# Kernel optimization log

Hardware: AMD Instinct MI355X
Metric: run time of the kernel (lower is better)

## Reference

```python
import jax, jax.numpy as jnp
import numpy as np

# ---- dimensions ----
N = 16384      # nodes
E = 131072     # edges (avg degree 8)
F = 128        # scalar channel width == s_dim
L = 9          # spherical-harmonic components (lmax=2)
R = 8          # radial basis size
DOUT = L * F   # post-product node width (1152)
K = 1024       # fixed number of master nodes (static stand-in for m>0.5)
HID = 64       # master-selection hidden dim
DA = 64        # virtual-attention head dim
LAMBDA_ATTN = 0.5
R_CUT = 5.0
EPS = 1e-9


def sh_l2(u):
    # real SH polynomials up to l=2 on unit vectors u[..., 3] -> [..., 9]
    x, y, z = u[..., 0], u[..., 1], u[..., 2]
    o = jnp.ones_like(x)
    return jnp.stack([o, x, y, z, x * y, y * z, 3.0 * z * z - 1.0, x * z, x * x - y * y], axis=-1)


def bessel(r):
    # Bessel radial basis; r [..., 1] -> [..., R]
    n = jnp.arange(1, R + 1, dtype=r.dtype)
    return jnp.sqrt(2.0 / R_CUT) * jnp.sin(n * jnp.pi * r / R_CUT) / jnp.maximum(r, EPS)


def setup_inputs() -> dict:
    key = jax.random.key(0)
    ks = jax.random.split(key, 18)
    s = lambda d: 1.0 / np.sqrt(d)
    return {
        'h': jax.random.normal(ks[0], (N, F), jnp.float32),
        'pos': 3.0 * jax.random.normal(ks[1], (N, 3), jnp.float32),
        'edge_sh': jax.random.normal(ks[2], (E, L), jnp.float32),
        'edge_feats': jax.random.uniform(ks[3], (E, R), jnp.float32),
        'W_node_l': s(F) * jax.random.normal(ks[4], (F, F), jnp.float32),
        'W_rad_l': s(R) * jax.random.normal(ks[5], (R, F), jnp.float32),
        'W_prod_l': s(L * F) * jax.random.normal(ks[6], (L, F, DOUT), jnp.float32),
        'ms_W1': s(F) * jax.random.normal(ks[7], (F, HID), jnp.float32),
        'ms_b1': jnp.zeros((HID,), jnp.float32),
        'ms_W2': s(HID) * jax.random.normal(ks[8], (HID, 1), jnp.float32),
        'ms_b2': jnp.zeros((1,), jnp.float32),
        'vg_Wq': s(F) * jax.random.normal(ks[9], (F, DA), jnp.float32),
        'vg_Wk': s(F) * jax.random.normal(ks[10], (F, DA), jnp.float32),
        'W_node_h': s(DOUT) * jax.random.normal(ks[11], (DOUT, F), jnp.float32),
        'W_rad_h': s(R) * jax.random.normal(ks[12], (R, F), jnp.float32),
        'W_prod_h': s(L * F) * jax.random.normal(ks[13], (L, F, DOUT), jnp.float32),
        'edge_index': jax.random.randint(ks[14], (2, E), 0, N),
    }


def reference(h, pos, edge_sh, edge_feats, W_node_l, W_rad_l, W_prod_l,
              ms_W1, ms_b1, ms_W2, ms_b2, vg_Wq, vg_Wk,
              W_node_h, W_rad_h, W_prod_h, edge_index):
    src, dst = edge_index[0], edge_index[1]

    # ---- local conv + reshape + prod (with padded residual sc) ----
    t = (h[src] @ W_node_l) * (edge_feats @ W_rad_l)                      # [E,F]
    msg = edge_sh[:, :, None] * t[:, None, :]                             # [E,L,F]
    upd = jax.ops.segment_sum(msg, dst, num_segments=N)                   # [N,L,F]
    sc = jnp.pad(h, ((0, 0), (0, DOUT - F)))
    h_local = jnp.einsum('nlf,lfg->ng', upd, W_prod_l) + sc               # [N,DOUT]

    # ---- master selection (MLP -> sigmoid); fixed top-K masters ----
    hs = h_local[:, :F]
    m = jax.nn.sigmoid(jax.nn.relu(hs @ ms_W1 + ms_b1) @ ms_W2 + ms_b2)[:, 0]  # [N]
    _, midx = jax.lax.top_k(m, K)
    master_idx = jnp.sort(midx)                                           # [K]

    # ---- induced subgraph among masters as dense [K,K] adjacency ----
    rank = jnp.full((N,), K, dtype=jnp.int32).at[master_idx].set(jnp.arange(K, dtype=jnp.int32))
    adj = jnp.zeros((K + 1, K + 1), h.dtype).at[rank[src], rank[dst]].max(jnp.ones((E,), h.dtype))
    adj_induced = adj[:K, :K]

    h_m = h_local[master_idx]                                             # [K,DOUT]
    pos_m = pos[master_idx]                                               # [K,3]
    hms = h_m[:, :F]

    # ---- virtual graph generation (attention -> thresholded dense adj) ----
    q = hms @ vg_Wq
    kk = hms @ vg_Wk
    A = jax.nn.sigmoid(q @ kk.T / jnp.sqrt(jnp.asarray(DA, h.dtype)))     # [K,K]
    A_virtual = jnp.where(A > LAMBDA_ATTN, A, 0.0)
    eye = jnp.eye(K, dtype=bool)
    Bv = (A_virtual > 0) & ~eye                                           # remove self loops
    Bv = Bv | Bv.T                                                        # to_undirected
    adj_master = jnp.clip(adj_induced + Bv.astype(h.dtype), 0.0, 1.0) * (1.0 - jnp.eye(K, dtype=h.dtype))

    # ---- hierarchical conv over dense master graph ----
    A_rec = adj_master.T                                                  # A_rec[i,j]=1: sender j -> receiver i
    V = pos_m[None, :, :] - pos_m[:, None, :]                             # vec = pos[src]-pos[dst]
    r = jnp.linalg.norm(V, axis=-1, keepdims=True)                        # [K,K,1]
    u = V / jnp.maximum(r, EPS)
    sh_m = sh_l2(u)                                                       # [K,K,L]
    rad = bessel(r)                                                       # [K,K,R]
    tm = (h_m @ W_node_h)[None, :, :] * (rad @ W_rad_h) * A_rec[:, :, None]  # [K,K,F]
    upd_m = jnp.einsum('ijl,ijf->ilf', sh_m, tm)                          # [K,L,F]
    h_hier = jnp.einsum('ilf,lfg->ig', upd_m, W_prod_h) + h_m             # sc_master pad is 0-width

    # ---- masked scatter blend ----
    h_exp = jnp.zeros_like(h_local).at[master_idx].set(h_hier)
    h_final = (1.0 - m[:, None]) * h_local + m[:, None] * h_exp
    return (h_final, A_virtual, m, master_idx)
```

## Files before the change

kernel.cpp:

```cpp
#include <hip/hip_runtime.h>
#include <hip/hip_bf16.h>
#include <stdint.h>

#define N_NODES 16384
#define E_EDGES 131072
#define F_DIM 128
#define L_DIM 9
#define R_DIM 8
#define DOUT_DIM 1152
#define K_SEL 1024
#define HID_DIM 64
#define DA_DIM 64

typedef unsigned short u16;
typedef __attribute__((ext_vector_type(8))) short bf16x8;
typedef __attribute__((ext_vector_type(4))) float f32x4;

static __device__ inline u16 f2bs(float x) {
  union { __hip_bfloat16 b; u16 s; } u;
  u.b = __float2bfloat16(x);
  return u.s;
}

#define GLDS16(gsrc, ldst) __builtin_amdgcn_global_load_lds( \
    (__attribute__((address_space(1))) void*)(void*)(gsrc),  \
    (__attribute__((address_space(3))) void*)(ldst), 16, 0, 0)

__global__ __launch_bounds__(256) void gemm_mfma(
    const float* __restrict__ A, const u16* __restrict__ Bt,
    float* __restrict__ C, int ldc, int M, int Nc, int Kc,
    const float* __restrict__ Add, int ldadd, int addW)
{
  __shared__ float Af[128 * 32];
  __shared__ u16  Bs[128 * 32];
  const int tid = threadIdx.x;
  const int wave = tid >> 6, lane = tid & 63;
  const int wm = wave >> 1, wn = wave & 1;
  const int l15 = lane & 15, quad = lane >> 4;
  const int bm = blockIdx.y * 128, bn = blockIdx.x * 128;

  f32x4 acc[4][4];
#pragma unroll
  for (int i = 0; i < 4; i++)
#pragma unroll
    for (int j = 0; j < 4; j++) acc[i][j] = (f32x4)(0.f);

  for (int k0 = 0; k0 < Kc; k0 += 32) {
    __syncthreads();
#pragma unroll
    for (int it = 0; it < 4; it++) {
      int c = it * 256 + tid;
      int row = c >> 3, op = c & 7;
      int oct = op ^ (row & 7);
      const float* g = A + (size_t)(bm + row) * Kc + k0 + oct * 4;
      GLDS16(g, &Af[c * 4]);
    }
#pragma unroll
    for (int it = 0; it < 2; it++) {
      int c = it * 256 + tid;
      int row = c >> 2, qp = c & 3;
      int q = qp ^ ((row >> 1) & 3);
      const u16* g = Bt + (size_t)(bn + row) * Kc + k0 + q * 8;
      GLDS16(g, &Bs[c * 8]);
    }
    __syncthreads();

    bf16x8 af[4], bfg[4];
#pragma unroll
    for (int mi = 0; mi < 4; mi++) {
      int m = wm * 64 + mi * 16 + l15;
      int o0 = (quad * 2) ^ (m & 7), o1 = (quad * 2 + 1) ^ (m & 7);
      float4 lo = *(const float4*)&Af[m * 32 + o0 * 4];
      float4 hi = *(const float4*)&Af[m * 32 + o1 * 4];
      bf16x8 r;
      r[0] = (short)f2bs(lo.x); r[1] = (short)f2bs(lo.y);
      r[2] = (short)f2bs(lo.z); r[3] = (short)f2bs(lo.w);
      r[4] = (short)f2bs(hi.x); r[5] = (short)f2bs(hi.y);
      r[6] = (short)f2bs(hi.z); r[7] = (short)f2bs(hi.w);
      af[mi] = r;
    }
#pragma unroll
    for (int ni = 0; ni < 4; ni++) {
      int n = wn * 64 + ni * 16 + l15;
      int q2 = quad ^ ((n >> 1) & 3);
      bfg[ni] = *(const bf16x8*)&Bs[n * 32 + q2 * 8];
    }
#pragma unroll
    for (int mi = 0; mi < 4; mi++)
#pragma unroll
      for (int ni = 0; ni < 4; ni++)
        acc[mi][ni] = __builtin_amdgcn_mfma_f32_16x16x32_bf16(af[mi], bfg[ni], acc[mi][ni], 0, 0, 0);
  }
#pragma unroll
  for (int mi = 0; mi < 4; mi++)
#pragma unroll
    for (int ni = 0; ni < 4; ni++)
#pragma unroll
      for (int r = 0; r < 4; r++) {
        int row = bm + wm * 64 + mi * 16 + quad * 4 + r;
        int col = bn + wn * 64 + ni * 16 + l15;
        float v = acc[mi][ni][r];
        if (Add != nullptr && col < addW) v += Add[(size_t)row * ldadd + col];
        C[(size_t)row * ldc + col] = v;
      }
}

__global__ __launch_bounds__(256) void gemm_mfma_b16(
    const u16* __restrict__ A, const u16* __restrict__ Bt,
    float* __restrict__ C, int ldc, int Kc, int nbx, int nwg,
    const float* __restrict__ Add, int ldadd, int addW)
{
  __shared__ u16 As[128 * 32];
  __shared__ u16 Bs[128 * 32];
  const int tid = threadIdx.x;
  const int wave = tid >> 6, lane = tid & 63;
  const int wm = wave >> 1, wn = wave & 1;
  const int l15 = lane & 15, quad = lane >> 4;
  const int lin = blockIdx.x;
  const int swz = (lin & 7) * (nwg >> 3) + (lin >> 3);
  const int bm = (swz / nbx) * 128, bn = (swz % nbx) * 128;

  f32x4 acc[4][4];
#pragma unroll
  for (int i = 0; i < 4; i++)
#pragma unroll
    for (int j = 0; j < 4; j++) acc[i][j] = (f32x4)(0.f);

  for (int k0 = 0; k0 < Kc; k0 += 32) {
    __syncthreads();
#pragma unroll
    for (int it = 0; it < 2; it++) {
      int c = it * 256 + tid;
      int row = c >> 2, qp = c & 3;
      int q = qp ^ ((row >> 1) & 3);
      const u16* g = A + (size_t)(bm + row) * Kc + k0 + q * 8;
      GLDS16(g, &As[c * 8]);
    }
#pragma unroll
    for (int it = 0; it < 2; it++) {
      int c = it * 256 + tid;
      int row = c >> 2, qp = c & 3;
      int q = qp ^ ((row >> 1) & 3);
      const u16* g = Bt + (size_t)(bn + row) * Kc + k0 + q * 8;
      GLDS16(g, &Bs[c * 8]);
    }
    __syncthreads();

    bf16x8 af[4], bfg[4];
#pragma unroll
    for (int mi = 0; mi < 4; mi++) {
      int m = wm * 64 + mi * 16 + l15;
      af[mi] = *(const bf16x8*)&As[m * 32 + (quad ^ ((m >> 1) & 3)) * 8];
    }
#pragma unroll
    for (int ni = 0; ni < 4; ni++) {
      int n = wn * 64 + ni * 16 + l15;
      bfg[ni] = *(const bf16x8*)&Bs[n * 32 + (quad ^ ((n >> 1) & 3)) * 8];
    }
#pragma unroll
    for (int mi = 0; mi < 4; mi++)
#pragma unroll
      for (int ni = 0; ni < 4; ni++)
        acc[mi][ni] = __builtin_amdgcn_mfma_f32_16x16x32_bf16(af[mi], bfg[ni], acc[mi][ni], 0, 0, 0);
  }
#pragma unroll
  for (int mi = 0; mi < 4; mi++)
#pragma unroll
    for (int ni = 0; ni < 4; ni++)
#pragma unroll
      for (int r = 0; r < 4; r++) {
        int row = bm + wm * 64 + mi * 16 + quad * 4 + r;
        int col = bn + wn * 64 + ni * 16 + l15;
        float v = acc[mi][ni][r];
        if (Add != nullptr && col < addW) v += Add[(size_t)row * ldadd + col];
        C[(size_t)row * ldc + col] = v;
      }
}

__global__ __launch_bounds__(256) void transpose_bf16(
    const float* __restrict__ W, u16* __restrict__ Bt, int K, int N)
{
  __shared__ float t[32][33];
  const int n0 = blockIdx.x * 32, k0 = blockIdx.y * 32;
  const int tx = threadIdx.x & 31, ty = threadIdx.x >> 5;
  for (int r = ty; r < 32; r += 8) t[r][tx] = W[(size_t)(k0 + r) * N + n0 + tx];
  __syncthreads();
  for (int r = ty; r < 32; r += 8) Bt[(size_t)(n0 + r) * K + k0 + tx] = f2bs(t[tx][r]);
}

#define BM 128
#define BN 128
#define BK 16
__global__ __launch_bounds__(256) void gemm_f32(
    const float* __restrict__ A, int lda,
    const float* __restrict__ B, int ldb,
    float* __restrict__ C, int ldc,
    int M, int Nc, int Kc,
    const float* __restrict__ Add, int ldadd, int addW)
{
  __shared__ float As[BK][BM + 1];
  __shared__ float Bs[BK][BN];
  const int tid = threadIdx.x;
  const int tx = tid & 15, ty = tid >> 4;
  const int bm = blockIdx.y * BM, bn = blockIdx.x * BN;
  float acc[8][8];
#pragma unroll
  for (int i = 0; i < 8; i++)
#pragma unroll
    for (int j = 0; j < 8; j++) acc[i][j] = 0.f;
  for (int k0 = 0; k0 < Kc; k0 += BK) {
    const int ac = tid & 15, ar0 = tid >> 4;
#pragma unroll
    for (int rr = 0; rr < 8; rr++) {
      int row = ar0 + rr * 16;
      As[ac][row] = A[(size_t)(bm + row) * lda + k0 + ac];
    }
    const int bc = tid & 127, br0 = tid >> 7;
#pragma unroll
    for (int rr = 0; rr < 8; rr++) {
      int kr = br0 + rr * 2;
      Bs[kr][bc] = B[(size_t)(k0 + kr) * ldb + bn + bc];
    }
    __syncthreads();
#pragma unroll
    for (int kk = 0; kk < BK; kk++) {
      float a[8], b[8];
#pragma unroll
      for (int i = 0; i < 8; i++) a[i] = As[kk][ty * 8 + i];
#pragma unroll
      for (int j = 0; j < 8; j++) b[j] = Bs[kk][tx * 8 + j];
#pragma unroll
      for (int i = 0; i < 8; i++)
#pragma unroll
        for (int j = 0; j < 8; j++) acc[i][j] = fmaf(a[i], b[j], acc[i][j]);
    }
    __syncthreads();
  }
#pragma unroll
  for (int i = 0; i < 8; i++) {
    int row = bm + ty * 8 + i;
#pragma unroll
    for (int j = 0; j < 8; j++) {
      int col = bn + tx * 8 + j;
      float v = acc[i][j];
      if (Add != nullptr && col < addW) v += Add[(size_t)row * ldadd + col];
      C[(size_t)row * ldc + col] = v;
    }
  }
}

__global__ __launch_bounds__(256) void gemm64_f32(
    const float* __restrict__ A, int lda,
    const float* __restrict__ B, int ldb,
    float* __restrict__ C, int ldc,
    int M, int Nc, int Kc, int kPerSplit,
    const float* __restrict__ Add, int ldadd, int addW)
{
  __shared__ float As[16][65];
  __shared__ float Bs[16][64];
  const int tid = threadIdx.x;
  const int tx = tid & 15, ty = tid >> 4;
  const int bm = blockIdx.y * 64, bn = blockIdx.x * 64;
  const int kb = blockIdx.z * kPerSplit;
  const int ke = min(kb + kPerSplit, Kc);
  float acc[4][4];
#pragma unroll
  for (int i = 0; i < 4; i++)
#pragma unroll
    for (int j = 0; j < 4; j++) acc[i][j] = 0.f;
  for (int k0 = kb; k0 < ke; k0 += 16) {
    const int ac = tid & 15, ar = tid >> 4;
#pragma unroll
    for (int rr = 0; rr < 4; rr++) {
      int row = ar + rr * 16;
      As[ac][row] = A[(size_t)(bm + row) * lda + k0 + ac];
    }
    const int bc = tid & 63, br = tid >> 6;
#pragma unroll
    for (int rr = 0; rr < 4; rr++) {
      int kr = br + rr * 4;
      Bs[kr][bc] = B[(size_t)(k0 + kr) * ldb + bn + bc];
    }
    __syncthreads();
#pragma unroll
    for (int kk = 0; kk < 16; kk++) {
      float a[4], b[4];
#pragma unroll
      for (int i = 0; i < 4; i++) a[i] = As[kk][ty * 4 + i];
#pragma unroll
      for (int j = 0; j < 4; j++) b[j] = Bs[kk][tx * 4 + j];
#pragma unroll
      for (int i = 0; i < 4; i++)
#pragma unroll
        for (int j = 0; j < 4; j++) acc[i][j] = fmaf(a[i], b[j], acc[i][j]);
    }
    __syncthreads();
  }
#pragma unroll
  for (int i = 0; i < 4; i++) {
    int row = bm + ty * 4 + i;
#pragma unroll
    for (int j = 0; j < 4; j++) {
      int col = bn + tx * 4 + j;
      if (gridDim.z > 1) {
        atomicAdd(&C[(size_t)row * ldc + col], acc[i][j]);
      } else {
        float v = acc[i][j];
        if (Add != nullptr && col < addW) v += Add[(size_t)row * ldadd + col];
        C[(size_t)row * ldc + col] = v;
      }
    }
  }
}

__global__ __launch_bounds__(256) void count_kernel(
    const int* __restrict__ ei, int* __restrict__ counts)
{
  int e = blockIdx.x * 256 + threadIdx.x;
  atomicAdd(&counts[ei[E_EDGES + e]], 1);
}

__global__ __launch_bounds__(1024) void scan_kernel(
    const int* __restrict__ counts, int* __restrict__ offsets, int* __restrict__ cursor)
{
  __shared__ int part[1024];
  const int t = threadIdx.x;
  const int base = t * 16;
  int loc[16];
  int s = 0;
#pragma unroll
  for (int k = 0; k < 16; k++) { loc[k] = counts[base + k]; s += loc[k]; }
  part[t] = s;
  __syncthreads();
  for (int d = 1; d < 1024; d <<= 1) {
    int v = (t >= d) ? part[t - d] : 0;
    __syncthreads();
    part[t] += v;
    __syncthreads();
  }
  int run = part[t] - s;
#pragma unroll
  for (int k = 0; k < 16; k++) {
    offsets[base + k] = run;
    cursor[base + k] = run;
    run += loc[k];
  }
}

__global__ __launch_bounds__(256) void fill_kernel(
    const int* __restrict__ ei, int* __restrict__ cursor, int* __restrict__ elist)
{
  int e = blockIdx.x * 256 + threadIdx.x;
  int d = ei[E_EDGES + e];
  int p = atomicAdd(&cursor[d], 1);
  elist[p] = e;
}

__global__ __launch_bounds__(128) void gather_accum_kernel(
    const float* __restrict__ hW, const float* __restrict__ edge_sh,
    const float* __restrict__ edge_feats, const float* __restrict__ W_rad_l,
    const int* __restrict__ ei, const int* __restrict__ offsets,
    const int* __restrict__ counts, const int* __restrict__ elist,
    float* __restrict__ upd, u16* __restrict__ updb)
{
  __shared__ float sWr[R_DIM * F_DIM];
  const int d = blockIdx.x, f = threadIdx.x;
  for (int t = f; t < R_DIM * F_DIM; t += 128) sWr[t] = W_rad_l[t];
  __syncthreads();
  const int b = offsets[d], n = counts[d];
  float acc[L_DIM];
#pragma unroll
  for (int l = 0; l < L_DIM; l++) acc[l] = 0.f;
  for (int k = 0; k < n; k++) {
    const int e = elist[b + k];
    const int s = ei[e];
    float rw = 0.f;
#pragma unroll
    for (int p = 0; p < R_DIM; p++)
      rw = fmaf(edge_feats[(size_t)e * R_DIM + p], sWr[p * F_DIM + f], rw);
    const float tf = hW[(size_t)s * F_DIM + f] * rw;
#pragma unroll
    for (int l = 0; l < L_DIM; l++)
      acc[l] = fmaf(edge_sh[(size_t)e * L_DIM + l], tf, acc[l]);
  }
#pragma unroll
  for (int l = 0; l < L_DIM; l++)
    upd[(size_t)d * DOUT_DIM + l * F_DIM + f] = acc[l];
  if (updb != nullptr) {
#pragma unroll
    for (int l = 0; l < L_DIM; l++)
      updb[(size_t)d * DOUT_DIM + l * F_DIM + f] = f2bs(acc[l]);
  }
}

__global__ __launch_bounds__(256) void gate_kernel(
    const float* __restrict__ hs, const float* __restrict__ W1,
    const float* __restrict__ b1, const float* __restrict__ W2,
    const float* __restrict__ b2, float* __restrict__ m_ws, float* __restrict__ m_out,
    int* __restrict__ hist1)
{
  __shared__ float sW1[F_DIM * HID_DIM];
  __shared__ float srow[4][F_DIM];
  const int tid = threadIdx.x;
  for (int t = tid; t < F_DIM * HID_DIM; t += 256) sW1[t] = W1[t];
  const int wave = tid >> 6, lane = tid & 63;
  const int n = blockIdx.x * 4 + wave;
  srow[wave][lane] = hs[(size_t)n * F_DIM + lane];
  srow[wave][lane + 64] = hs[(size_t)n * F_DIM + lane + 64];
  __syncthreads();
  float hid = b1[lane];
#pragma unroll 8
  for (int c = 0; c < F_DIM; c++) hid = fmaf(srow[wave][c], sW1[c * HID_DIM + lane], hid);
  hid = fmaxf(hid, 0.f);
  float v = hid * W2[lane];
#pragma unroll
  for (int off = 32; off > 0; off >>= 1) v += __shfl_down(v, off);
  if (lane == 0) {
    float mm = 1.f / (1.f + expf(-(v + b2[0])));
    m_ws[n] = mm;
    m_out[n] = mm;
    unsigned mb = __float_as_uint(mm);
    atomicAdd(&hist1[mb >> 16], 1);
  }
}

__global__ __launch_bounds__(1024) void radix_sel_kernel(
    const int* __restrict__ hist, const int* __restrict__ kin, int kinIdx,
    int* __restrict__ outp, int outIdx)
{
  __shared__ int part[1024];
  const int t = threadIdx.x;
  const int Kv = kin ? kin[kinIdx] : K_SEL;
  const int base = t * 64;
  int s = 0;
  for (int k = 0; k < 64; k++) s += hist[base + k];
  part[t] = s;
  __syncthreads();
  for (int d = 1; d < 1024; d <<= 1) {
    int v = (t + d < 1024) ? part[t + d] : 0;
    __syncthreads();
    part[t] += v;
    __syncthreads();
  }
  int inc = part[t];
  if (inc >= Kv && inc - s < Kv) {
    int r = inc - s;
    for (int b = base + 63; b >= base; b--) {
      int hv = hist[b];
      if (r + hv >= Kv) { outp[outIdx] = b; outp[outIdx + 1] = Kv - r; break; }
      r += hv;
    }
  }
}

__global__ __launch_bounds__(256) void hist2_kernel(
    const float* __restrict__ m_ws, const int* __restrict__ selb, int* __restrict__ hist2)
{
  int i = blockIdx.x * 256 + threadIdx.x;
  unsigned mb = __float_as_uint(m_ws[i]);
  if ((int)(mb >> 16) == selb[0]) atomicAdd(&hist2[mb & 0xFFFFu], 1);
}

__global__ __launch_bounds__(256) void flag_kernel(
    const float* __restrict__ m_ws, int* __restrict__ selb,
    unsigned char* __restrict__ flags, int* __restrict__ cand)
{
  int i = blockIdx.x * 256 + threadIdx.x;
  unsigned mb = __float_as_uint(m_ws[i]);
  unsigned vb = ((unsigned)selb[0] << 16) | (unsigned)selb[2];
  unsigned char fl = 0;
  if (mb > vb) fl = 1;
  else if (mb == vb) { int p = atomicAdd(&selb[4], 1); cand[p] = i; }
  flags[i] = fl;
}

__global__ __launch_bounds__(1024) void cand_kernel(
    const int* __restrict__ selb, const int* __restrict__ cand, unsigned char* __restrict__ flags)
{
  const int nc = selb[4], need = selb[3];
  for (int c = threadIdx.x; c < nc; c += 1024) {
    const int idx = cand[c];
    int r = 0;
    for (int o = 0; o < nc; o++) r += (cand[o] < idx) ? 1 : 0;
    if (r < need) flags[idx] = 1;
  }
}

__global__ __launch_bounds__(1024) void compact_kernel(
    const unsigned char* __restrict__ flags, int* __restrict__ midx,
    int* __restrict__ rank, float* __restrict__ mi_out)
{
  __shared__ int part[1024];
  const int t = threadIdx.x;
  const int base = t * 16;
  int loc[16];
  int s = 0;
#pragma unroll
  for (int k = 0; k < 16; k++) { loc[k] = flags[base + k]; s += loc[k]; }
  part[t] = s;
  __syncthreads();
  for (int d = 1; d < 1024; d <<= 1) {
    int v = (t >= d) ? part[t - d] : 0;
    __syncthreads();
    part[t] += v;
    __syncthreads();
  }
  int run = part[t] - s;
#pragma unroll
  for (int k = 0; k < 16; k++) {
    int i = base + k;
    if (loc[k]) {
      midx[run] = i;
      mi_out[run] = (float)i;
      rank[i] = run;
      run++;
    } else {
      rank[i] = K_SEL;
    }
  }
}

__global__ __launch_bounds__(256) void adj_kernel(
    const int* __restrict__ ei, const int* __restrict__ rank, unsigned char* __restrict__ adjm)
{
  int e = blockIdx.x * 256 + threadIdx.x;
  int rs = rank[ei[e]];
  int rd = rank[ei[E_EDGES + e]];
  if (rs < K_SEL && rd < K_SEL) adjm[(size_t)rs * K_SEL + rd] = 1;
}

__global__ __launch_bounds__(128) void gather_kernel(
    const float* __restrict__ hl, const float* __restrict__ pos,
    const int* __restrict__ midx, float* __restrict__ h_m, float* __restrict__ pos_m)
{
  const int rI = blockIdx.x, t = threadIdx.x;
  const int mi = midx[rI];
  const float4* src = (const float4*)(hl + (size_t)mi * DOUT_DIM);
  float4* dst = (float4*)(h_m + (size_t)rI * DOUT_DIM);
  for (int c = t; c < DOUT_DIM / 4; c += 128) dst[c] = src[c];
  if (t < 3) pos_m[rI * 3 + t] = pos[mi * 3 + t];
}

__global__ __launch_bounds__(128) void qk_kernel(
    const float* __restrict__ hs, const int* __restrict__ midx,
    const float* __restrict__ Wq, const float* __restrict__ Wk,
    float* __restrict__ q, float* __restrict__ kk)
{
  __shared__ float row[F_DIM];
  const int i = blockIdx.x, t = threadIdx.x;
  const int mi = midx[i];
  row[t] = hs[(size_t)mi * F_DIM + t];
  __syncthreads();
  const int d = t & 63;
  const float* W = (t < 64) ? Wq : Wk;
  float acc = 0.f;
#pragma unroll 8
  for (int c = 0; c < F_DIM; c++) acc = fmaf(row[c], W[c * DA_DIM + d], acc);
  float* dst = (t < 64) ? q : kk;
  dst[(size_t)i * DA_DIM + d] = acc;
}

__global__ __launch_bounds__(256) void attn_kernel(
    const float* __restrict__ q, const float* __restrict__ kk,
    unsigned char* __restrict__ maskA, float* __restrict__ Av)
{
  __shared__ float qs[16][DA_DIM], ks[16][DA_DIM];
  const int tx = threadIdx.x, ty = threadIdx.y;
  const int tid = ty * 16 + tx;
  const int i0 = blockIdx.y * 16, j0 = blockIdx.x * 16;
  for (int t = tid; t < 16 * DA_DIM; t += 256) {
    int rr = t >> 6, cc = t & 63;
    qs[rr][cc] = q[(size_t)(i0 + rr) * DA_DIM + cc];
    ks[rr][cc] = kk[(size_t)(j0 + rr) * DA_DIM + cc];
  }
  __syncthreads();
  float acc = 0.f;
#pragma unroll
  for (int d2 = 0; d2 < DA_DIM; d2++) acc = fmaf(qs[ty][d2], ks[tx][d2], acc);
  float sgl = 1.f / (1.f + expf(-acc * 0.125f));
  size_t o = (size_t)(i0 + ty) * K_SEL + (j0 + tx);
  bool big = sgl > 0.5f;
  maskA[o] = big ? 1 : 0;
  Av[o] = big ? sgl : 0.f;
}

__global__ __launch_bounds__(256) void listbuild_kernel(
    const unsigned char* __restrict__ adjm, const unsigned char* __restrict__ maskA,
    u16* __restrict__ list, int* __restrict__ nj)
{
  __shared__ int cnt;
  const int i = blockIdx.x, tid = threadIdx.x;
  if (tid == 0) cnt = 0;
  __syncthreads();
#pragma unroll
  for (int jt = 0; jt < 4; jt++) {
    int j = jt * 256 + tid;
    bool e = (j != i) && (adjm[(size_t)j * K_SEL + i] | maskA[(size_t)j * K_SEL + i] |
                          maskA[(size_t)i * K_SEL + j]);
    if (e) {
      int p = atomicAdd(&cnt, 1);
      list[(size_t)i * K_SEL + p] = (u16)j;
    }
  }
  __syncthreads();
  if (tid == 0) nj[i] = cnt;
}

__global__ __launch_bounds__(512) void hier2_kernel(
    const float* __restrict__ hWn, const float* __restrict__ pos_m,
    const float* __restrict__ W_rad_h, const u16* __restrict__ list,
    const int* __restrict__ nj, float* __restrict__ upd_m, u16* __restrict__ updb_m)
{
  __shared__ float sW[R_DIM * F_DIM];
  __shared__ float gsm[128][20];
  __shared__ int sj[128];
  __shared__ float red[3][L_DIM][F_DIM];
  const int tid = threadIdx.x;
  const int i = blockIdx.x;
  const int f = tid & 127, jsub = tid >> 7;
  for (int t = tid; t < R_DIM * F_DIM; t += 512) sW[t] = W_rad_h[t];
  const float pix = pos_m[i * 3 + 0], piy = pos_m[i * 3 + 1], piz = pos_m[i * 3 + 2];
  float acc[L_DIM];
#pragma unroll
  for (int l = 0; l < L_DIM; l++) acc[l] = 0.f;
  const int n = nj[i];
  for (int c0 = 0; c0 < n; c0 += 128) {
    const int cnt = min(128, n - c0);
    __syncthreads();
    if (tid < cnt) {
      const int j = list[(size_t)i * K_SEL + c0 + tid];
      sj[tid] = j;
      float vx = pos_m[j * 3 + 0] - pix;
      float vy = pos_m[j * 3 + 1] - piy;
      float vz = pos_m[j * 3 + 2] - piz;
      float r = sqrtf(vx * vx + vy * vy + vz * vz);
      float rm = fmaxf(r, 1e-9f);
      float inv = 1.f / rm;
      float ux = vx * inv, uy = vy * inv, uz = vz * inv;
      gsm[tid][0] = 1.f; gsm[tid][1] = ux; gsm[tid][2] = uy; gsm[tid][3] = uz;
      gsm[tid][4] = ux * uy; gsm[tid][5] = uy * uz;
      gsm[tid][6] = 3.f * uz * uz - 1.f;
      gsm[tid][7] = ux * uz; gsm[tid][8] = ux * ux - uy * uy;
      float theta = 0.62831853071795864769f * r;
      float s1 = sinf(theta), c1 = cosf(theta);
      float coef = 0.632455532033675866f * inv;
      float snm2 = 0.f, snm1 = s1;
      gsm[tid][9] = s1 * coef;
#pragma unroll
      for (int nn = 2; nn <= R_DIM; nn++) {
        float sn = 2.f * c1 * snm1 - snm2;
        gsm[tid][8 + nn] = sn * coef;
        snm2 = snm1; snm1 = sn;
      }
      gsm[tid][17] = 0.f; gsm[tid][18] = 0.f; gsm[tid][19] = 0.f;
    }
    __syncthreads();
    for (int t = jsub; t < cnt; t += 4) {
      const int j = sj[t];
      const float hw = hWn[(size_t)j * F_DIM + f];
      float4 g0 = *(const float4*)&gsm[t][0];
      float4 g1 = *(const float4*)&gsm[t][4];
      float4 g2 = *(const float4*)&gsm[t][8];
      float4 g3 = *(const float4*)&gsm[t][12];
      float  g4 = gsm[t][16];
      float rw = g2.y * sW[0 * F_DIM + f];
      rw = fmaf(g2.z, sW[1 * F_DIM + f], rw);
      rw = fmaf(g2.w, sW[2 * F_DIM + f], rw);
      rw = fmaf(g3.x, sW[3 * F_DIM + f], rw);
      rw = fmaf(g3.y, sW[4 * F_DIM + f], rw);
      rw = fmaf(g3.z, sW[5 * F_DIM + f], rw);
      rw = fmaf(g3.w, sW[6 * F_DIM + f], rw);
      rw = fmaf(g4,   sW[7 * F_DIM + f], rw);
      const float tm = hw * rw;
      acc[0] = fmaf(g0.x, tm, acc[0]); acc[1] = fmaf(g0.y, tm, acc[1]);
      acc[2] = fmaf(g0.z, tm, acc[2]); acc[3] = fmaf(g0.w, tm, acc[3]);
      acc[4] = fmaf(g1.x, tm, acc[4]); acc[5] = fmaf(g1.y, tm, acc[5]);
      acc[6] = fmaf(g1.z, tm, acc[6]); acc[7] = fmaf(g1.w, tm, acc[7]);
      acc[8] = fmaf(g2.x, tm, acc[8]);
    }
  }
  __syncthreads();
  if (jsub > 0) {
#pragma unroll
    for (int l = 0; l < L_DIM; l++) red[jsub - 1][l][f] = acc[l];
  }
  __syncthreads();
  if (jsub == 0) {
#pragma unroll
    for (int l = 0; l < L_DIM; l++) {
      float v = acc[l] + red[0][l][f] + red[1][l][f] + red[2][l][f];
      upd_m[(size_t)i * DOUT_DIM + l * F_DIM + f] = v;
      updb_m[(size_t)i * DOUT_DIM + l * F_DIM + f] = f2bs(v);
    }
  }
}

__global__ __launch_bounds__(256) void combine_kernel(
    float* __restrict__ out0, const float* __restrict__ h_hier,
    const float* __restrict__ m_ws, const int* __restrict__ rank)
{
  size_t i4 = (size_t)blockIdx.x * 256 + threadIdx.x;
  int n = (int)(i4 / (DOUT_DIM / 4));
  int g4 = (int)(i4 % (DOUT_DIM / 4));
  float mv = m_ws[n];
  int r = rank[n];
  float4 hl = ((const float4*)out0)[i4];
  float4 he = make_float4(0.f, 0.f, 0.f, 0.f);
  if (r < K_SEL) he = ((const float4*)h_hier)[(size_t)r * (DOUT_DIM / 4) + g4];
  float4 o;
  o.x = (1.f - mv) * hl.x + mv * he.x;
  o.y = (1.f - mv) * hl.y + mv * he.y;
  o.z = (1.f - mv) * hl.z + mv * he.z;
  o.w = (1.f - mv) * hl.w + mv * he.w;
  ((float4*)out0)[i4] = o;
}

extern "C" void kernel_launch(void* const* d_in, const int* in_sizes, int n_in,
                              void* d_out, int out_size, void* d_ws, size_t ws_size,
                              hipStream_t stream)
{
  const float* h         = (const float*)d_in[0];
  const float* pos       = (const float*)d_in[1];
  const float* edge_sh   = (const float*)d_in[2];
  const float* edge_feats= (const float*)d_in[3];
  const float* W_node_l  = (const float*)d_in[4];
  const float* W_rad_l   = (const float*)d_in[5];
  const float* W_prod_l  = (const float*)d_in[6];
  const float* ms_W1     = (const float*)d_in[7];
  const float* ms_b1     = (const float*)d_in[8];
  const float* ms_W2     = (const float*)d_in[9];
  const float* ms_b2     = (const float*)d_in[10];
  const float* vg_Wq     = (const float*)d_in[11];
  const float* vg_Wk     = (const float*)d_in[12];
  const float* W_node_h  = (const float*)d_in[13];
  const float* W_rad_h   = (const float*)d_in[14];
  const float* W_prod_h  = (const float*)d_in[15];
  const int*   eidx      = (const int*)d_in[16];

  float* out    = (float*)d_out;
  float* out_hf = out;
  float* out_Av = out + (size_t)N_NODES * DOUT_DIM;
  float* out_m  = out_Av + (size_t)K_SEL * K_SEL;
  float* out_mi = out_m + N_NODES;

  char* ws = (char*)d_ws;
  float* upd = (float*)ws;
  float* hW  = (float*)(ws + (size_t)N_NODES * DOUT_DIM * 4);
  float* hs  = hW;
  const size_t updbOff = (size_t)N_NODES * DOUT_DIM * 4 + (size_t)N_NODES * F_DIM * 4;
  const size_t updbNeed = updbOff + (size_t)N_NODES * DOUT_DIM * 2;
  const bool useB16 = (ws_size >= updbNeed);
  u16* updb = (u16*)(ws + updbOff);
  u16* Btl = (u16*)out_Av;
  char* csr = (char*)out_Av + (((size_t)DOUT_DIM * DOUT_DIM * 2 + 255) & ~(size_t)255);
  int* counts  = (int*)csr;
  int* offsets = counts + N_NODES;
  int* cursor  = offsets + N_NODES;
  int* elist   = cursor + N_NODES;
  size_t off = 0;
  auto alloc = [&](size_t bytes) -> void* {
    void* p = ws + off;
    off += (bytes + 255) & ~(size_t)255;
    return p;
  };
  float* m_ws  = (float*)alloc((size_t)N_NODES * 4);
  int*   rank  = (int*)alloc((size_t)N_NODES * 4);
  int*   midx  = (int*)alloc((size_t)K_SEL * 4);
  int*   hist1 = (int*)alloc((size_t)65536 * 4);
  int*   hist2 = (int*)alloc((size_t)65536 * 4);
  int*   selb  = (int*)alloc((size_t)64 * 4);
  int*   cand  = (int*)alloc((size_t)N_NODES * 4);
  unsigned char* flags = (unsigned char*)alloc((size_t)N_NODES);
  unsigned char* adjm  = (unsigned char*)alloc((size_t)K_SEL * K_SEL);
  unsigned char* maskA = (unsigned char*)alloc((size_t)K_SEL * K_SEL);
  float* qbuf  = (float*)alloc((size_t)K_SEL * DA_DIM * 4);
  float* kbuf  = (float*)alloc((size_t)K_SEL * DA_DIM * 4);
  float* h_m   = (float*)alloc((size_t)K_SEL * DOUT_DIM * 4);
  float* pos_m = (float*)alloc((size_t)K_SEL * 3 * 4);
  float* hWn   = (float*)alloc((size_t)K_SEL * F_DIM * 4);
  float* upd_m = (float*)alloc((size_t)K_SEL * DOUT_DIM * 4);
  float* h_hier= (float*)alloc((size_t)K_SEL * DOUT_DIM * 4);
  u16*   Bth   = (u16*)alloc((size_t)DOUT_DIM * DOUT_DIM * 2);
  u16*   jlist = (u16*)alloc((size_t)K_SEL * K_SEL * 2);
  int*   njbuf = (int*)alloc((size_t)K_SEL * 4);
  u16*   updbm = (u16*)alloc((size_t)K_SEL * DOUT_DIM * 2);

  hipMemsetAsync(counts, 0, (size_t)N_NODES * 4, stream);
  transpose_bf16<<<dim3(DOUT_DIM / 32, DOUT_DIM / 32), 256, 0, stream>>>(
      W_prod_l, Btl, DOUT_DIM, DOUT_DIM);
  gemm_f32<<<dim3(1, N_NODES / 128), 256, 0, stream>>>(
      h, F_DIM, W_node_l, F_DIM, hW, F_DIM, N_NODES, F_DIM, F_DIM, nullptr, 0, 0);
  count_kernel<<<E_EDGES / 256, 256, 0, stream>>>(eidx, counts);
  scan_kernel<<<1, 1024, 0, stream>>>(counts, offsets, cursor);
  fill_kernel<<<E_EDGES / 256, 256, 0, stream>>>(eidx, cursor, elist);
  gather_accum_kernel<<<N_NODES, 128, 0, stream>>>(
      hW, edge_sh, edge_feats, W_rad_l, eidx, offsets, counts, elist, upd,
      useB16 ? updb : nullptr);
  gemm64_f32<<<dim3(F_DIM / 64, N_NODES / 64, 1), 256, 0, stream>>>(
      upd, DOUT_DIM, W_prod_l, DOUT_DIM, hs, F_DIM,
      N_NODES, F_DIM, DOUT_DIM, DOUT_DIM, h, F_DIM, F_DIM);
  if (useB16) {
    gemm_mfma_b16<<<(DOUT_DIM / 128) * (N_NODES / 128), 256, 0, stream>>>(
        updb, Btl, out_hf, DOUT_DIM, DOUT_DIM, DOUT_DIM / 128,
        (DOUT_DIM / 128) * (N_NODES / 128), h, F_DIM, F_DIM);
  } else {
    gemm_mfma<<<dim3(DOUT_DIM / 128, N_NODES / 128), 256, 0, stream>>>(
        upd, Btl, out_hf, DOUT_DIM, N_NODES, DOUT_DIM, DOUT_DIM, h, F_DIM, F_DIM);
  }

  hipMemsetAsync(adjm, 0, (size_t)K_SEL * K_SEL, stream);
  hipMemsetAsync(hist1, 0, (size_t)65536 * 4 * 2 + 256, stream);
  transpose_bf16<<<dim3(DOUT_DIM / 32, DOUT_DIM / 32), 256, 0, stream>>>(
      W_prod_h, Bth, DOUT_DIM, DOUT_DIM);
  gate_kernel<<<N_NODES / 4, 256, 0, stream>>>(hs, ms_W1, ms_b1, ms_W2, ms_b2,
                                               m_ws, out_m, hist1);
  radix_sel_kernel<<<1, 1024, 0, stream>>>(hist1, nullptr, 0, selb, 0);
  hist2_kernel<<<N_NODES / 256, 256, 0, stream>>>(m_ws, selb, hist2);
  radix_sel_kernel<<<1, 1024, 0, stream>>>(hist2, selb, 1, selb, 2);
  flag_kernel<<<N_NODES / 256, 256, 0, stream>>>(m_ws, selb, flags, cand);
  cand_kernel<<<1, 1024, 0, stream>>>(selb, cand, flags);
  compact_kernel<<<1, 1024, 0, stream>>>(flags, midx, rank, out_mi);
  adj_kernel<<<E_EDGES / 256, 256, 0, stream>>>(eidx, rank, adjm);
  gather_kernel<<<K_SEL, 128, 0, stream>>>(out_hf, pos, midx, h_m, pos_m);
  qk_kernel<<<K_SEL, 128, 0, stream>>>(hs, midx, vg_Wq, vg_Wk, qbuf, kbuf);
  attn_kernel<<<dim3(K_SEL / 16, K_SEL / 16), dim3(16, 16), 0, stream>>>(qbuf, kbuf, maskA, out_Av);
  listbuild_kernel<<<K_SEL, 256, 0, stream>>>(adjm, maskA, jlist, njbuf);
  hipMemsetAsync(hWn, 0, (size_t)K_SEL * F_DIM * 4, stream);
  gemm64_f32<<<dim3(F_DIM / 64, K_SEL / 64, 4), 256, 0, stream>>>(
      h_m, DOUT_DIM, W_node_h, F_DIM, hWn, F_DIM,
      K_SEL, F_DIM, DOUT_DIM, DOUT_DIM / 4, nullptr, 0, 0);
  hier2_kernel<<<K_SEL, 512, 0, stream>>>(hWn, pos_m, W_rad_h, jlist, njbuf, upd_m, updbm);
  gemm_mfma_b16<<<(DOUT_DIM / 128) * (K_SEL / 128), 256, 0, stream>>>(
      updbm, Bth, h_hier, DOUT_DIM, DOUT_DIM, DOUT_DIM / 128,
      (DOUT_DIM / 128) * (K_SEL / 128), h_m, DOUT_DIM, DOUT_DIM);
  combine_kernel<<<(N_NODES * DOUT_DIM / 4) / 256, 256, 0, stream>>>(out_hf, h_hier, m_ws, rank);
}
```

Before: 734.2 us.

## Split-K the hs projection GEMM with 128x128 tiles and a reduce pass

Replaces the 64x64-tile fp32 GEMM that computes hs (the first 128 output columns, using upd and W_prod_l) with a 128x128-tile kernel split four ways along K. Partial sums go to the not-yet-written output buffer, and a separate vectorized kernel sums the four partials and adds the h residual. The small h@W_node_l GEMM now uses the 64x64 kernel instead of the 128-tile one, which gives it more blocks. The split-K path is meant to raise per-thread reuse and parallelism, and in exchange adds an extra 32 MB write and read of partials and one more launch.

```diff
diff --git a/kernel.cpp b/kernel.cpp
--- a/kernel.cpp
+++ b/kernel.cpp
@@ -188,42 +188,39 @@
   for (int r = ty; r < 32; r += 8) Bt[(size_t)(n0 + r) * K + k0 + tx] = f2bs(t[tx][r]);
 }
 
-#define BM 128
-#define BN 128
-#define BK 16
-__global__ __launch_bounds__(256) void gemm_f32(
-    const float* __restrict__ A, int lda,
-    const float* __restrict__ B, int ldb,
-    float* __restrict__ C, int ldc,
-    int M, int Nc, int Kc,
-    const float* __restrict__ Add, int ldadd, int addW)
-{
-  __shared__ float As[BK][BM + 1];
-  __shared__ float Bs[BK][BN];
+__global__ __launch_bounds__(256) void hs_gemm_kernel(
+    const float* __restrict__ A,
+    const float* __restrict__ B,
+    float* __restrict__ psum)
+{
+  __shared__ float As[16][129];
+  __shared__ float Bs[16][128];
   const int tid = threadIdx.x;
   const int tx = tid & 15, ty = tid >> 4;
-  const int bm = blockIdx.y * BM, bn = blockIdx.x * BN;
+  const int bm = blockIdx.x * 128;
+  const int z = blockIdx.y;
+  const int kb = z * (DOUT_DIM / 4);
   float acc[8][8];
 #pragma unroll
   for (int i = 0; i < 8; i++)
 #pragma unroll
     for (int j = 0; j < 8; j++) acc[i][j] = 0.f;
-  for (int k0 = 0; k0 < Kc; k0 += BK) {
+  for (int k0 = kb; k0 < kb + DOUT_DIM / 4; k0 += 16) {
     const int ac = tid & 15, ar0 = tid >> 4;
 #pragma unroll
     for (int rr = 0; rr < 8; rr++) {
       int row = ar0 + rr * 16;
-      As[ac][row] = A[(size_t)(bm + row) * lda + k0 + ac];
+      As[ac][row] = A[(size_t)(bm + row) * DOUT_DIM + k0 + ac];
     }
     const int bc = tid & 127, br0 = tid >> 7;
 #pragma unroll
     for (int rr = 0; rr < 8; rr++) {
       int kr = br0 + rr * 2;
-      Bs[kr][bc] = B[(size_t)(k0 + kr) * ldb + bn + bc];
-    }
-    __syncthreads();
-#pragma unroll
-    for (int kk = 0; kk < BK; kk++) {
+      Bs[kr][bc] = B[(size_t)(k0 + kr) * DOUT_DIM + bc];
+    }
+    __syncthreads();
+#pragma unroll
+    for (int kk = 0; kk < 16; kk++) {
       float a[8], b[8];
 #pragma unroll
       for (int i = 0; i < 8; i++) a[i] = As[kk][ty * 8 + i];
@@ -238,15 +235,27 @@
   }
 #pragma unroll
   for (int i = 0; i < 8; i++) {
-    int row = bm + ty * 8 + i;
-#pragma unroll
-    for (int j = 0; j < 8; j++) {
-      int col = bn + tx * 8 + j;
-      float v = acc[i][j];
-      if (Add != nullptr && col < addW) v += Add[(size_t)row * ldadd + col];
-      C[(size_t)row * ldc + col] = v;
-    }
-  }
+    size_t row = (size_t)z * N_NODES + bm + ty * 8 + i;
+#pragma unroll
+    for (int j = 0; j < 8; j++)
+      psum[row * F_DIM + tx * 8 + j] = acc[i][j];
+  }
+}
+
+__global__ __launch_bounds__(256) void hs_reduce_kernel(
+    const float* __restrict__ psum, const float* __restrict__ h, float* __restrict__ hs)
+{
+  size_t i4 = (size_t)blockIdx.x * 256 + threadIdx.x;
+  const size_t stride = (size_t)N_NODES * F_DIM / 4;
+  const float4* p = (const float4*)psum;
+  float4 a = p[i4], b = p[i4 + stride], c = p[i4 + 2 * stride], d = p[i4 + 3 * stride];
+  float4 hh = ((const float4*)h)[i4];
+  float4 o;
+  o.x = a.x + b.x + c.x + d.x + hh.x;
+  o.y = a.y + b.y + c.y + d.y + hh.y;
+  o.z = a.z + b.z + c.z + d.z + hh.z;
+  o.w = a.w + b.w + c.w + d.w + hh.w;
+  ((float4*)hs)[i4] = o;
 }
 
 __global__ __launch_bounds__(256) void gemm64_f32(
@@ -751,6 +760,7 @@
   const size_t updbNeed = updbOff + (size_t)N_NODES * DOUT_DIM * 2;
   const bool useB16 = (ws_size >= updbNeed);
   u16* updb = (u16*)(ws + updbOff);
+  float* psum = out_hf;
   u16* Btl = (u16*)out_Av;
   char* csr = (char*)out_Av + (((size_t)DOUT_DIM * DOUT_DIM * 2 + 255) & ~(size_t)255);
   int* counts  = (int*)csr;
@@ -788,17 +798,16 @@
   hipMemsetAsync(counts, 0, (size_t)N_NODES * 4, stream);
   transpose_bf16<<<dim3(DOUT_DIM / 32, DOUT_DIM / 32), 256, 0, stream>>>(
       W_prod_l, Btl, DOUT_DIM, DOUT_DIM);
-  gemm_f32<<<dim3(1, N_NODES / 128), 256, 0, stream>>>(
-      h, F_DIM, W_node_l, F_DIM, hW, F_DIM, N_NODES, F_DIM, F_DIM, nullptr, 0, 0);
+  gemm64_f32<<<dim3(F_DIM / 64, N_NODES / 64, 1), 256, 0, stream>>>(
+      h, F_DIM, W_node_l, F_DIM, hW, F_DIM, N_NODES, F_DIM, F_DIM, F_DIM, nullptr, 0, 0);
   count_kernel<<<E_EDGES / 256, 256, 0, stream>>>(eidx, counts);
   scan_kernel<<<1, 1024, 0, stream>>>(counts, offsets, cursor);
   fill_kernel<<<E_EDGES / 256, 256, 0, stream>>>(eidx, cursor, elist);
   gather_accum_kernel<<<N_NODES, 128, 0, stream>>>(
       hW, edge_sh, edge_feats, W_rad_l, eidx, offsets, counts, elist, upd,
       useB16 ? updb : nullptr);
-  gemm64_f32<<<dim3(F_DIM / 64, N_NODES / 64, 1), 256, 0, stream>>>(
-      upd, DOUT_DIM, W_prod_l, DOUT_DIM, hs, F_DIM,
-      N_NODES, F_DIM, DOUT_DIM, DOUT_DIM, h, F_DIM, F_DIM);
+  hs_gemm_kernel<<<dim3(N_NODES / 128, 4), 256, 0, stream>>>(upd, W_prod_l, psum);
+  hs_reduce_kernel<<<(N_NODES * F_DIM / 4) / 256, 256, 0, stream>>>(psum, h, hs);
   if (useB16) {
     gemm_mfma_b16<<<(DOUT_DIM / 128) * (N_NODES / 128), 256, 0, stream>>>(
         updb, Btl, out_hf, DOUT_DIM, DOUT_DIM, DOUT_DIM / 128,
```

After: 716.7 us. 2.4% less time.
